# Kernel optimization log

Measured on AMD Instinct MI355X. Metric: run time of the kernel, lower is better.

Reference implementation:

```python
import jax, jax.numpy as jnp
import numpy as np

N = 100000
E = 1250000
H = 64


def setup_inputs() -> dict:
    key = jax.random.key(0)
    ks = jax.random.split(key, 20)
    x = jax.random.normal(ks[0], (N, 1), dtype=jnp.float32)
    edge_index = jax.random.randint(ks[1], (2, E), 0, N, dtype=jnp.int64)
    edge_attr = jax.random.uniform(ks[2], (E,), dtype=jnp.float32)
    def lin(k, fin, fout):
        s = 1.0 / np.sqrt(fin)
        kw, kb = jax.random.split(k)
        W = jax.random.uniform(kw, (fin, fout), minval=-s, maxval=s, dtype=jnp.float32)
        b = jax.random.uniform(kb, (fout,), minval=-s, maxval=s, dtype=jnp.float32)
        return W, b
    W1, b1 = lin(ks[3], 1, H)
    W2, b2 = lin(ks[4], H, H)
    W3, b3 = lin(ks[5], H, H)
    W4, b4 = lin(ks[6], H, H)
    W5, b5 = lin(ks[7], H, H)
    fW1, fb1 = lin(ks[8], H, H)
    fW2, fb2 = lin(ks[9], H, 1)
    return dict(x=x, edge_index=edge_index, edge_attr=edge_attr,
                W1=W1, b1=b1, W2=W2, b2=b2, W3=W3, b3=b3, W4=W4, b4=b4,
                W5=W5, b5=b5, fW1=fW1, fb1=fb1, fW2=fW2, fb2=fb2)


def _gcn_layer(x, W, b, src, dst, ew):
    # PyG GCNConv: x' = D^{-1/2}(A+I)D^{-1/2} x W + b (self-loops pre-appended)
    h = x @ W                                   # [N, H]
    deg = jax.ops.segment_sum(ew, dst, num_segments=N)
    dinv = jnp.where(deg > 0, jax.lax.rsqrt(deg), 0.0)
    norm = dinv[src] * ew * dinv[dst]           # [E+N]
    msg = h[src] * norm[:, None]                # [E+N, H]
    return jax.ops.segment_sum(msg, dst, num_segments=N) + b


def reference(x, edge_index, edge_attr, W1, b1, W2, b2, W3, b3, W4, b4, W5, b5, fW1, fb1, fW2, fb2):
    loops = jnp.arange(N, dtype=edge_index.dtype)
    src = jnp.concatenate([edge_index[0], loops])
    dst = jnp.concatenate([edge_index[1], loops])
    ew = jnp.concatenate([edge_attr, jnp.ones((N,), edge_attr.dtype)])
    h = jax.nn.relu(_gcn_layer(x, W1, b1, src, dst, ew))
    h = jax.nn.relu(_gcn_layer(h, W2, b2, src, dst, ew))
    h = jax.nn.relu(_gcn_layer(h, W3, b3, src, dst, ew))
    h = jax.nn.relu(_gcn_layer(h, W4, b4, src, dst, ew))
    h = jax.nn.relu(_gcn_layer(h, W5, b5, src, dst, ew))
    h = jax.nn.relu(h @ fW1 + fb1)
    return h @ fW2 + fb2
```

## Files before the change

kernel.cpp:

```cpp
#include <hip/hip_runtime.h>
#include <hip/hip_bf16.h>

#define NN 100000
#define EE 1250000

#define RL(x, l) __builtin_amdgcn_readlane((x), (l))
#define RLF(x, l) __int_as_float(__builtin_amdgcn_readlane(__float_as_int(x), (l)))

typedef __attribute__((ext_vector_type(8))) short v8s;
typedef __attribute__((ext_vector_type(4))) float v4f;
typedef __attribute__((ext_vector_type(4))) unsigned int v4u;

__device__ __forceinline__ unsigned short bf16rtn(float x) {
    unsigned u = __float_as_uint(x);
    unsigned r = u + 0x7fffu + ((u >> 16) & 1u);
    return (unsigned short)(r >> 16);
}
__device__ __forceinline__ unsigned bf16rtn2(float lo, float hi) {
    return (unsigned)bf16rtn(lo) | ((unsigned)bf16rtn(hi) << 16);
}
__device__ __forceinline__ float bflo(unsigned u) { return __uint_as_float(u << 16); }
__device__ __forceinline__ float bfhi(unsigned u) { return __uint_as_float(u & 0xffff0000u); }
__device__ __forceinline__ float bfs(unsigned short s) { return __uint_as_float((unsigned)s << 16); }


__global__ __launch_bounds__(256) void k_count(const int* __restrict__ ei,
                                               const float* __restrict__ ew,
                                               unsigned long long* __restrict__ cnt,
                                               int* __restrict__ slot) {
    int e = blockIdx.x * 256 + threadIdx.x;
    if (e >= EE) return;
    int d = __builtin_nontemporal_load(&ei[EE + e]);
    float w = __builtin_nontemporal_load(&ew[e]);
    unsigned fx = (unsigned)(w * 16777216.0f + 0.5f);
    unsigned long long old =
        atomicAdd(&cnt[d], (1ULL << 32) | (unsigned long long)fx);
    __builtin_nontemporal_store((int)(old >> 32), &slot[e]);
}

__global__ __launch_bounds__(256) void k_bsum(const unsigned long long* __restrict__ cnt,
                                              int* __restrict__ bsum) {
    __shared__ int ls[256];
    int b = blockIdx.x, tid = threadIdx.x;
    int base = b * 1024 + tid * 4;
    int s = 0;
    #pragma unroll
    for (int j = 0; j < 4; ++j) { int g = base + j; if (g < NN) s += (int)(cnt[g] >> 32); }
    ls[tid] = s; __syncthreads();
    for (int off = 128; off > 0; off >>= 1) {
        if (tid < off) ls[tid] += ls[tid + off];
        __syncthreads();
    }
    if (tid == 0) bsum[b] = ls[0];
}

__global__ __launch_bounds__(256) void k_scan_out(const unsigned long long* __restrict__ cnt,
                                                  const int* __restrict__ bsum,
                                                  const float* __restrict__ x,
                                                  int* __restrict__ rowptr,
                                                  float* __restrict__ dinv,
                                                  float* __restrict__ xd) {
    __shared__ int ls[256];
    __shared__ int sbase;
    int b = blockIdx.x, tid = threadIdx.x;
    if (tid < 64) {
        int w0 = (tid < b) ? bsum[tid] : 0;
        int w1 = ((64 + tid) < b) ? bsum[64 + tid] : 0;
        int s = w0 + w1;
        #pragma unroll
        for (int m = 32; m >= 1; m >>= 1) s += __shfl_xor(s, m, 64);
        if (tid == 0) sbase = s;
    }
    int base = b * 1024 + tid * 4;
    int c[4]; float sw[4]; int s = 0;
    #pragma unroll
    for (int j = 0; j < 4; ++j) {
        int g = base + j;
        unsigned long long v = (g < NN) ? cnt[g] : 0ULL;
        c[j] = (int)(v >> 32);
        sw[j] = (float)(unsigned)(v & 0xffffffffu) * (1.0f / 16777216.0f);
        s += c[j];
    }
    ls[tid] = s; __syncthreads();
    for (int off = 1; off < 256; off <<= 1) {
        int v = (tid >= off) ? ls[tid - off] : 0;
        __syncthreads();
        ls[tid] += v;
        __syncthreads();
    }
    int excl = ls[tid] - s + sbase;
    #pragma unroll
    for (int j = 0; j < 4; ++j) {
        int g = base + j;
        if (g < NN) {
            rowptr[g + 1] = excl + c[j];
            excl += c[j];
            float di = rsqrtf(sw[j] + 1.0f);
            dinv[g] = di;
            xd[g] = di * x[g];
        }
    }
    if (b == 0 && tid == 0) rowptr[0] = 0;
}

__global__ __launch_bounds__(256) void k_fill(const int* __restrict__ ei,
                                              const float* __restrict__ ew,
                                              const int* __restrict__ slot,
                                              const int* __restrict__ rowptr,
                                              int2* __restrict__ epair) {
    int e = blockIdx.x * 256 + threadIdx.x;
    if (e >= EE) return;
    int s = __builtin_nontemporal_load(&ei[e]);
    int d = __builtin_nontemporal_load(&ei[EE + e]);
    float w = __builtin_nontemporal_load(&ew[e]);
    int sl = __builtin_nontemporal_load(&slot[e]);
    int p = rowptr[d] + sl;
    epair[p] = make_int2(s, __float_as_int(w));
}

__global__ __launch_bounds__(256) void k_wpk(const float* __restrict__ Wa,
                                             const float* __restrict__ Wb,
                                             const float* __restrict__ Wc,
                                             const float* __restrict__ Wd,
                                             unsigned* __restrict__ Wf) {
    const float* W = (blockIdx.x == 0) ? Wa : (blockIdx.x == 1) ? Wb
                   : (blockIdx.x == 2) ? Wc : Wd;
    unsigned* out = Wf + blockIdx.x * 4096;
    int t = threadIdx.x;
    #pragma unroll
    for (int i = 0; i < 2; ++i) {
        int s = t * 2 + i;
        int lane = s & 63;
        int nt = (s >> 6) & 3;
        int kt = s >> 8;
        int col = nt * 16 + (lane & 15);
        int k0 = kt * 32 + (lane >> 4) * 8;
        unsigned hi[4], lo[4];
        #pragma unroll
        for (int d = 0; d < 4; ++d) {
            float w0 = W[(k0 + 2 * d) * 64 + col];
            float w1 = W[(k0 + 2 * d + 1) * 64 + col];
            unsigned short h0 = bf16rtn(w0), h1 = bf16rtn(w1);
            float r0 = w0 - bfs(h0), r1 = w1 - bfs(h1);
            hi[d] = (unsigned)h0 | ((unsigned)h1 << 16);
            lo[d] = (unsigned)bf16rtn(r0) | ((unsigned)bf16rtn(r1) << 16);
        }
        int gh = (0 * 2 + kt) * 4 + nt;
        int gl = (1 * 2 + kt) * 4 + nt;
        *(v4u*)&out[(gh * 64 + lane) * 4] = (v4u){hi[0], hi[1], hi[2], hi[3]};
        *(v4u*)&out[(gl * 64 + lane) * 4] = (v4u){lo[0], lo[1], lo[2], lo[3]};
    }
}

__device__ __forceinline__ void gatherq(
    const unsigned* __restrict__ G16, const int2* __restrict__ ep,
    int node, int beg, int end, int l16,
    float& a0, float& a1, float& a2, float& a3)
{
    uint2 su = *(const uint2*)&G16[node * 32 + l16 * 2];
    a0 = bflo(su.x); a1 = bfhi(su.x);
    a2 = bflo(su.y); a3 = bfhi(su.y);
    int j = beg;
    for (; j + 8 <= end; j += 8) {
        uint2 u[8]; float nv[8];
        #pragma unroll
        for (int t = 0; t < 8; ++t) {
            int2 p = ep[j + t];
            nv[t] = __int_as_float(p.y);
            u[t] = *(const uint2*)&G16[p.x * 32 + l16 * 2];
        }
        #pragma unroll
        for (int t = 0; t < 8; ++t) {
            a0 = fmaf(bflo(u[t].x), nv[t], a0);
            a1 = fmaf(bfhi(u[t].x), nv[t], a1);
            a2 = fmaf(bflo(u[t].y), nv[t], a2);
            a3 = fmaf(bfhi(u[t].y), nv[t], a3);
        }
    }
    if (j < end) {
        uint2 u[8]; float nv[8];
        #pragma unroll
        for (int t = 0; t < 8; ++t) {
            int idx = j + t;
            int2 p = ep[idx < end ? idx : j];
            nv[t] = (idx < end) ? __int_as_float(p.y) : 0.f;
            u[t] = *(const uint2*)&G16[p.x * 32 + l16 * 2];
        }
        #pragma unroll
        for (int t = 0; t < 8; ++t) {
            a0 = fmaf(bflo(u[t].x), nv[t], a0);
            a1 = fmaf(bfhi(u[t].x), nv[t], a1);
            a2 = fmaf(bflo(u[t].y), nv[t], a2);
            a3 = fmaf(bfhi(u[t].y), nv[t], a3);
        }
    }
}


__global__ __launch_bounds__(256) void k_l1(
    const float* __restrict__ xd, const float* __restrict__ dinv,
    const int* __restrict__ rowptr, const int2* __restrict__ ep,
    const float* __restrict__ W1, const float* __restrict__ b1,
    const float* __restrict__ W2, unsigned short* __restrict__ Gout)
{
    __shared__ float sW[4096];
    int tid = threadIdx.x;
    #pragma unroll
    for (int i = 0; i < 16; ++i) sW[tid + i * 256] = W2[tid + i * 256];
    __syncthreads();
    int lane = tid & 63, l16 = lane & 15, sub = lane >> 4;
    int g4 = blockIdx.x * 4 + (tid >> 6);
    int nodeS = g4 * 4 + sub;
    int beg = rowptr[nodeS], end = rowptr[nodeS + 1];
    float partial = 0.f;
    for (int idx = beg + l16; idx < end; idx += 16) {
        int2 p = ep[idx];
        partial = fmaf(__int_as_float(p.y), xd[p.x], partial);
    }
    #pragma unroll
    for (int m = 8; m >= 1; m >>= 1) partial += __shfl_xor(partial, m, 64);
    float z = dinv[nodeS] * (xd[nodeS] + partial);
    float z0 = RLF(z, 0), z1 = RLF(z, 16), z2 = RLF(z, 32), z3 = RLF(z, 48);
    float w1l = W1[lane], b1l = b1[lane];
    float v0 = fmaxf(fmaf(z0, w1l, b1l), 0.f);
    float v1 = fmaxf(fmaf(z1, w1l, b1l), 0.f);
    float v2 = fmaxf(fmaf(z2, w1l, b1l), 0.f);
    float v3 = fmaxf(fmaf(z3, w1l, b1l), 0.f);
    float a0 = 0.f, a1 = 0.f, a2 = 0.f, a3 = 0.f;
    #pragma unroll
    for (int k = 0; k < 64; ++k) {
        float wk = sW[k * 64 + lane];
        a0 = fmaf(RLF(v0, k), wk, a0);
        a1 = fmaf(RLF(v1, k), wk, a1);
        a2 = fmaf(RLF(v2, k), wk, a2);
        a3 = fmaf(RLF(v3, k), wk, a3);
    }
    int n0 = g4 * 4;
    Gout[(n0 + 0) * 64 + lane] = bf16rtn(dinv[n0 + 0] * a0);
    Gout[(n0 + 1) * 64 + lane] = bf16rtn(dinv[n0 + 1] * a1);
    Gout[(n0 + 2) * 64 + lane] = bf16rtn(dinv[n0 + 2] * a2);
    Gout[(n0 + 3) * 64 + lane] = bf16rtn(dinv[n0 + 3] * a3);
}

__global__ __launch_bounds__(256) void k_gmv(
    const unsigned* __restrict__ G16, const float* __restrict__ dinv,
    const int* __restrict__ rowptr, const int2* __restrict__ ep,
    const float* __restrict__ bias, const unsigned* __restrict__ Wf,
    unsigned short* __restrict__ Gout)
{
    __shared__ __align__(16) unsigned sB[4096];
    __shared__ __align__(16) unsigned sA[4][128];
    int tid = threadIdx.x;
    #pragma unroll
    for (int i = 0; i < 4; ++i)
        ((v4u*)sB)[tid + i * 256] = ((const v4u*)Wf)[tid + i * 256];
    int lane = tid & 63;
    int wid  = tid >> 6;
    int q    = lane >> 4;
    int l16  = lane & 15;
    int n0 = (blockIdx.x * 4 + wid) * 4;
    int node = n0 + q;
    int beg = rowptr[node], end = rowptr[node + 1];
    float a0, a1, a2, a3;
    gatherq(G16, ep, node, beg, end, l16, a0, a1, a2, a3);
    float din = dinv[node];
    float4 bv = *(const float4*)&bias[l16 * 4];
    float v0 = fmaxf(fmaf(din, a0, bv.x), 0.f);
    float v1 = fmaxf(fmaf(din, a1, bv.y), 0.f);
    float v2 = fmaxf(fmaf(din, a2, bv.z), 0.f);
    float v3 = fmaxf(fmaf(din, a3, bv.w), 0.f);
    *(uint2*)&sA[wid][q * 32 + l16 * 2] =
        make_uint2(bf16rtn2(v0, v1), bf16rtn2(v2, v3));
    __syncthreads();
    int rr  = lane & 3;
    int blk = lane >> 4;
    v8s fa0 = *(const v8s*)&sA[wid][rr * 32 +  0 + blk * 4];
    v8s fa1 = *(const v8s*)&sA[wid][rr * 32 + 16 + blk * 4];
    v4f acc[4];
    #pragma unroll
    for (int nt = 0; nt < 4; ++nt) {
        v8s bh0 = *(const v8s*)&sB[((0 * 4 + nt) * 64 + lane) * 4];
        v8s bh1 = *(const v8s*)&sB[((1 * 4 + nt) * 64 + lane) * 4];
        v8s bl0 = *(const v8s*)&sB[((2 * 4 + nt) * 64 + lane) * 4];
        v8s bl1 = *(const v8s*)&sB[((3 * 4 + nt) * 64 + lane) * 4];
        v4f c = {0.f, 0.f, 0.f, 0.f};
        c = __builtin_amdgcn_mfma_f32_16x16x32_bf16(fa0, bl0, c, 0, 0, 0);
        c = __builtin_amdgcn_mfma_f32_16x16x32_bf16(fa1, bl1, c, 0, 0, 0);
        c = __builtin_amdgcn_mfma_f32_16x16x32_bf16(fa0, bh0, c, 0, 0, 0);
        c = __builtin_amdgcn_mfma_f32_16x16x32_bf16(fa1, bh1, c, 0, 0, 0);
        acc[nt] = c;
    }
    if (lane < 16) {
        float4 dn = *(const float4*)&dinv[n0];
        #pragma unroll
        for (int r = 0; r < 4; ++r) {
            float d = (r == 0) ? dn.x : (r == 1) ? dn.y : (r == 2) ? dn.z : dn.w;
            #pragma unroll
            for (int nt = 0; nt < 4; ++nt)
                Gout[(n0 + r) * 64 + nt * 16 + lane] = bf16rtn(d * acc[nt][r]);
        }
    }
}

__global__ __launch_bounds__(256) void k_ghead(
    const unsigned* __restrict__ G16, const float* __restrict__ dinv,
    const int* __restrict__ rowptr, const int2* __restrict__ ep,
    const float* __restrict__ b5, const unsigned* __restrict__ Wf,
    const float* __restrict__ fb1, const float* __restrict__ fW2,
    const float* __restrict__ fb2, float* __restrict__ out)
{
    __shared__ __align__(16) unsigned sB[4096];
    __shared__ __align__(16) unsigned sA[4][128];
    int tid = threadIdx.x;
    #pragma unroll
    for (int i = 0; i < 4; ++i)
        ((v4u*)sB)[tid + i * 256] = ((const v4u*)Wf)[tid + i * 256];
    int lane = tid & 63;
    int wid  = tid >> 6;
    int q    = lane >> 4;
    int l16  = lane & 15;
    int n0 = (blockIdx.x * 4 + wid) * 4;
    int node = n0 + q;
    float fb1v[4], fw2v[4];
    #pragma unroll
    for (int nt = 0; nt < 4; ++nt) {
        fb1v[nt] = fb1[nt * 16 + l16];
        fw2v[nt] = fW2[nt * 16 + l16];
    }
    float fb2s = fb2[0];
    int beg = rowptr[node], end = rowptr[node + 1];
    float a0, a1, a2, a3;
    gatherq(G16, ep, node, beg, end, l16, a0, a1, a2, a3);
    float din = dinv[node];
    float4 bv = *(const float4*)&b5[l16 * 4];
    float v0 = fmaxf(fmaf(din, a0, bv.x), 0.f);
    float v1 = fmaxf(fmaf(din, a1, bv.y), 0.f);
    float v2 = fmaxf(fmaf(din, a2, bv.z), 0.f);
    float v3 = fmaxf(fmaf(din, a3, bv.w), 0.f);
    *(uint2*)&sA[wid][q * 32 + l16 * 2] =
        make_uint2(bf16rtn2(v0, v1), bf16rtn2(v2, v3));
    __syncthreads();
    int rr  = lane & 3;
    int blk = lane >> 4;
    v8s fa0 = *(const v8s*)&sA[wid][rr * 32 +  0 + blk * 4];
    v8s fa1 = *(const v8s*)&sA[wid][rr * 32 + 16 + blk * 4];
    v4f acc[4];
    #pragma unroll
    for (int nt = 0; nt < 4; ++nt) {
        v8s bh0 = *(const v8s*)&sB[((0 * 4 + nt) * 64 + lane) * 4];
        v8s bh1 = *(const v8s*)&sB[((1 * 4 + nt) * 64 + lane) * 4];
        v8s bl0 = *(const v8s*)&sB[((2 * 4 + nt) * 64 + lane) * 4];
        v8s bl1 = *(const v8s*)&sB[((3 * 4 + nt) * 64 + lane) * 4];
        v4f c = {0.f, 0.f, 0.f, 0.f};
        c = __builtin_amdgcn_mfma_f32_16x16x32_bf16(fa0, bl0, c, 0, 0, 0);
        c = __builtin_amdgcn_mfma_f32_16x16x32_bf16(fa1, bl1, c, 0, 0, 0);
        c = __builtin_amdgcn_mfma_f32_16x16x32_bf16(fa0, bh0, c, 0, 0, 0);
        c = __builtin_amdgcn_mfma_f32_16x16x32_bf16(fa1, bh1, c, 0, 0, 0);
        acc[nt] = c;
    }
    float tr[4];
    #pragma unroll
    for (int r = 0; r < 4; ++r) {
        float t = 0.f;
        #pragma unroll
        for (int nt = 0; nt < 4; ++nt)
            t += fmaxf(acc[nt][r] + fb1v[nt], 0.f) * fw2v[nt];
        #pragma unroll
        for (int m = 8; m >= 1; m >>= 1) t += __shfl_xor(t, m, 64);
        tr[r] = t;
    }
    if (lane == 0) {
        float4 o = {tr[0] + fb2s, tr[1] + fb2s, tr[2] + fb2s, tr[3] + fb2s};
        *(float4*)&out[n0] = o;
    }
}


extern "C" void kernel_launch(void* const* d_in, const int* in_sizes, int n_in,
                              void* d_out, int out_size, void* d_ws, size_t ws_size,
                              hipStream_t stream) {
    const float* x   = (const float*)d_in[0];
    const int*   ei  = (const int*)d_in[1];
    const float* ew  = (const float*)d_in[2];
    const float* W1  = (const float*)d_in[3];
    const float* b1  = (const float*)d_in[4];
    const float* W2  = (const float*)d_in[5];
    const float* b2  = (const float*)d_in[6];
    const float* W3  = (const float*)d_in[7];
    const float* b3  = (const float*)d_in[8];
    const float* W4  = (const float*)d_in[9];
    const float* b4  = (const float*)d_in[10];
    const float* W5  = (const float*)d_in[11];
    const float* b5  = (const float*)d_in[12];
    const float* fW1 = (const float*)d_in[13];
    const float* fb1 = (const float*)d_in[14];
    const float* fW2 = (const float*)d_in[15];
    const float* fb2 = (const float*)d_in[16];
    float* out = (float*)d_out;

    char* ws = (char*)d_ws;
    size_t o = 0;
    auto alloc = [&](size_t elems) -> void* {
        void* p = (void*)(ws + o);
        o += ((elems * 4 + 255) / 256) * 256;
        return p;
    };
    float* dinv   = (float*)alloc(NN);
    float* xd     = (float*)alloc(NN);
    int*   rowptr = (int*)alloc(NN + 1);
    unsigned long long* cnt64 = (unsigned long long*)alloc(2 * (size_t)NN);
    int*   bsum   = (int*)alloc(128);
    int2*  epair  = (int2*)alloc(2 * (size_t)EE);
    unsigned* Ga16 = (unsigned*)alloc((size_t)NN * 32);
    unsigned* Gb16 = (unsigned*)alloc((size_t)NN * 32);
    int*   slot   = (int*)alloc(EE);
    unsigned* Wf  = (unsigned*)alloc(4 * 4096);

    int gE  = (EE + 255) / 256;
    int nb  = (NN + 1023) / 1024;
    int gW4 = NN / 16;

    k_wpk<<<4, 256, 0, stream>>>(W3, W4, W5, fW1, Wf);
    hipMemsetAsync(cnt64, 0, NN * sizeof(unsigned long long), stream);
    k_count<<<gE, 256, 0, stream>>>(ei, ew, cnt64, slot);
    k_bsum<<<nb, 256, 0, stream>>>(cnt64, bsum);
    k_scan_out<<<nb, 256, 0, stream>>>(cnt64, bsum, x, rowptr, dinv, xd);
    k_fill<<<gE, 256, 0, stream>>>(ei, ew, slot, rowptr, epair);

    k_l1<<<gW4, 256, 0, stream>>>(xd, dinv, rowptr, epair, W1, b1, W2,
                                  (unsigned short*)Ga16);
    k_gmv<<<gW4, 256, 0, stream>>>(Ga16, dinv, rowptr, epair, b2, Wf + 0,
                                   (unsigned short*)Gb16);
    k_gmv<<<gW4, 256, 0, stream>>>(Gb16, dinv, rowptr, epair, b3, Wf + 4096,
                                   (unsigned short*)Ga16);
    k_gmv<<<gW4, 256, 0, stream>>>(Ga16, dinv, rowptr, epair, b4, Wf + 8192,
                                   (unsigned short*)Gb16);
    k_ghead<<<gW4, 256, 0, stream>>>(Gb16, dinv, rowptr, epair, b5, Wf + 12288,
                                     fb1, fW2, fb2, out);
}
```

Measured before the change: 399.7 us.

## Gather 8 nodes per wavefront with 16-byte row loads in GCN layers

```diff
diff --git a/kernel.cpp b/kernel.cpp
--- a/kernel.cpp
+++ b/kernel.cpp
@@ -152,46 +152,55 @@
     }
 }
 
-__device__ __forceinline__ void gatherq(
+__device__ __forceinline__ void gatherq8(
     const unsigned* __restrict__ G16, const int2* __restrict__ ep,
-    int node, int beg, int end, int l16,
-    float& a0, float& a1, float& a2, float& a3)
+    int node, int beg, int end, int l8, float a[8])
 {
-    uint2 su = *(const uint2*)&G16[node * 32 + l16 * 2];
-    a0 = bflo(su.x); a1 = bfhi(su.x);
-    a2 = bflo(su.y); a3 = bfhi(su.y);
+    uint4 su = *(const uint4*)&G16[node * 32 + l8 * 4];
+    a[0] = bflo(su.x); a[1] = bfhi(su.x);
+    a[2] = bflo(su.y); a[3] = bfhi(su.y);
+    a[4] = bflo(su.z); a[5] = bfhi(su.z);
+    a[6] = bflo(su.w); a[7] = bfhi(su.w);
     int j = beg;
     for (; j + 8 <= end; j += 8) {
-        uint2 u[8]; float nv[8];
+        uint4 u[8]; float nv[8];
         #pragma unroll
         for (int t = 0; t < 8; ++t) {
             int2 p = ep[j + t];
             nv[t] = __int_as_float(p.y);
-            u[t] = *(const uint2*)&G16[p.x * 32 + l16 * 2];
+            u[t] = *(const uint4*)&G16[p.x * 32 + l8 * 4];
         }
         #pragma unroll
         for (int t = 0; t < 8; ++t) {
-            a0 = fmaf(bflo(u[t].x), nv[t], a0);
-            a1 = fmaf(bfhi(u[t].x), nv[t], a1);
-            a2 = fmaf(bflo(u[t].y), nv[t], a2);
-            a3 = fmaf(bfhi(u[t].y), nv[t], a3);
+            a[0] = fmaf(bflo(u[t].x), nv[t], a[0]);
+            a[1] = fmaf(bfhi(u[t].x), nv[t], a[1]);
+            a[2] = fmaf(bflo(u[t].y), nv[t], a[2]);
+            a[3] = fmaf(bfhi(u[t].y), nv[t], a[3]);
+            a[4] = fmaf(bflo(u[t].z), nv[t], a[4]);
+            a[5] = fmaf(bfhi(u[t].z), nv[t], a[5]);
+            a[6] = fmaf(bflo(u[t].w), nv[t], a[6]);
+            a[7] = fmaf(bfhi(u[t].w), nv[t], a[7]);
         }
     }
     if (j < end) {
-        uint2 u[8]; float nv[8];
+        uint4 u[8]; float nv[8];
         #pragma unroll
         for (int t = 0; t < 8; ++t) {
             int idx = j + t;
             int2 p = ep[idx < end ? idx : j];
             nv[t] = (idx < end) ? __int_as_float(p.y) : 0.f;
-            u[t] = *(const uint2*)&G16[p.x * 32 + l16 * 2];
+            u[t] = *(const uint4*)&G16[p.x * 32 + l8 * 4];
         }
         #pragma unroll
         for (int t = 0; t < 8; ++t) {
-            a0 = fmaf(bflo(u[t].x), nv[t], a0);
-            a1 = fmaf(bfhi(u[t].x), nv[t], a1);
-            a2 = fmaf(bflo(u[t].y), nv[t], a2);
-            a3 = fmaf(bfhi(u[t].y), nv[t], a3);
+            a[0] = fmaf(bflo(u[t].x), nv[t], a[0]);
+            a[1] = fmaf(bfhi(u[t].x), nv[t], a[1]);
+            a[2] = fmaf(bflo(u[t].y), nv[t], a[2]);
+            a[3] = fmaf(bfhi(u[t].y), nv[t], a[3]);
+            a[4] = fmaf(bflo(u[t].z), nv[t], a[4]);
+            a[5] = fmaf(bfhi(u[t].z), nv[t], a[5]);
+            a[6] = fmaf(bflo(u[t].w), nv[t], a[6]);
+            a[7] = fmaf(bfhi(u[t].w), nv[t], a[7]);
         }
     }
 }
@@ -249,30 +258,36 @@
     unsigned short* __restrict__ Gout)
 {
     __shared__ __align__(16) unsigned sB[4096];
-    __shared__ __align__(16) unsigned sA[4][128];
+    __shared__ __align__(16) unsigned sA[4][256];
     int tid = threadIdx.x;
     #pragma unroll
     for (int i = 0; i < 4; ++i)
         ((v4u*)sB)[tid + i * 256] = ((const v4u*)Wf)[tid + i * 256];
     int lane = tid & 63;
     int wid  = tid >> 6;
-    int q    = lane >> 4;
-    int l16  = lane & 15;
-    int n0 = (blockIdx.x * 4 + wid) * 4;
+    int q    = lane >> 3;
+    int l8   = lane & 7;
+    int n0 = (blockIdx.x * 4 + wid) * 8;
     int node = n0 + q;
     int beg = rowptr[node], end = rowptr[node + 1];
-    float a0, a1, a2, a3;
-    gatherq(G16, ep, node, beg, end, l16, a0, a1, a2, a3);
+    float a[8];
+    gatherq8(G16, ep, node, beg, end, l8, a);
     float din = dinv[node];
-    float4 bv = *(const float4*)&bias[l16 * 4];
-    float v0 = fmaxf(fmaf(din, a0, bv.x), 0.f);
-    float v1 = fmaxf(fmaf(din, a1, bv.y), 0.f);
-    float v2 = fmaxf(fmaf(din, a2, bv.z), 0.f);
-    float v3 = fmaxf(fmaf(din, a3, bv.w), 0.f);
-    *(uint2*)&sA[wid][q * 32 + l16 * 2] =
-        make_uint2(bf16rtn2(v0, v1), bf16rtn2(v2, v3));
+    float4 bv0 = ((const float4*)bias)[l8 * 2];
+    float4 bv1 = ((const float4*)bias)[l8 * 2 + 1];
+    float v0 = fmaxf(fmaf(din, a[0], bv0.x), 0.f);
+    float v1 = fmaxf(fmaf(din, a[1], bv0.y), 0.f);
+    float v2 = fmaxf(fmaf(din, a[2], bv0.z), 0.f);
+    float v3 = fmaxf(fmaf(din, a[3], bv0.w), 0.f);
+    float v4 = fmaxf(fmaf(din, a[4], bv1.x), 0.f);
+    float v5 = fmaxf(fmaf(din, a[5], bv1.y), 0.f);
+    float v6 = fmaxf(fmaf(din, a[6], bv1.z), 0.f);
+    float v7 = fmaxf(fmaf(din, a[7], bv1.w), 0.f);
+    *(uint4*)&sA[wid][q * 32 + l8 * 4] = make_uint4(
+        bf16rtn2(v0, v1), bf16rtn2(v2, v3),
+        bf16rtn2(v4, v5), bf16rtn2(v6, v7));
     __syncthreads();
-    int rr  = lane & 3;
+    int rr  = lane & 7;
     int blk = lane >> 4;
     v8s fa0 = *(const v8s*)&sA[wid][rr * 32 +  0 + blk * 4];
     v8s fa1 = *(const v8s*)&sA[wid][rr * 32 + 16 + blk * 4];
@@ -290,14 +305,17 @@
         c = __builtin_amdgcn_mfma_f32_16x16x32_bf16(fa1, bh1, c, 0, 0, 0);
         acc[nt] = c;
     }
-    if (lane < 16) {
-        float4 dn = *(const float4*)&dinv[n0];
+    int grp = lane >> 4;
+    int l16 = lane & 15;
+    if (grp < 2) {
+        int rb = grp * 4;
+        float4 dn = *(const float4*)&dinv[n0 + rb];
         #pragma unroll
         for (int r = 0; r < 4; ++r) {
             float d = (r == 0) ? dn.x : (r == 1) ? dn.y : (r == 2) ? dn.z : dn.w;
             #pragma unroll
             for (int nt = 0; nt < 4; ++nt)
-                Gout[(n0 + r) * 64 + nt * 16 + lane] = bf16rtn(d * acc[nt][r]);
+                Gout[(n0 + rb + r) * 64 + nt * 16 + l16] = bf16rtn(d * acc[nt][r]);
         }
     }
 }
@@ -310,16 +328,17 @@
     const float* __restrict__ fb2, float* __restrict__ out)
 {
     __shared__ __align__(16) unsigned sB[4096];
-    __shared__ __align__(16) unsigned sA[4][128];
+    __shared__ __align__(16) unsigned sA[4][256];
     int tid = threadIdx.x;
     #pragma unroll
     for (int i = 0; i < 4; ++i)
         ((v4u*)sB)[tid + i * 256] = ((const v4u*)Wf)[tid + i * 256];
     int lane = tid & 63;
     int wid  = tid >> 6;
-    int q    = lane >> 4;
+    int q    = lane >> 3;
+    int l8   = lane & 7;
     int l16  = lane & 15;
-    int n0 = (blockIdx.x * 4 + wid) * 4;
+    int n0 = (blockIdx.x * 4 + wid) * 8;
     int node = n0 + q;
     float fb1v[4], fw2v[4];
     #pragma unroll
@@ -329,18 +348,24 @@
     }
     float fb2s = fb2[0];
     int beg = rowptr[node], end = rowptr[node + 1];
-    float a0, a1, a2, a3;
-    gatherq(G16, ep, node, beg, end, l16, a0, a1, a2, a3);
+    float a[8];
+    gatherq8(G16, ep, node, beg, end, l8, a);
     float din = dinv[node];
-    float4 bv = *(const float4*)&b5[l16 * 4];
-    float v0 = fmaxf(fmaf(din, a0, bv.x), 0.f);
-    float v1 = fmaxf(fmaf(din, a1, bv.y), 0.f);
-    float v2 = fmaxf(fmaf(din, a2, bv.z), 0.f);
-    float v3 = fmaxf(fmaf(din, a3, bv.w), 0.f);
-    *(uint2*)&sA[wid][q * 32 + l16 * 2] =
-        make_uint2(bf16rtn2(v0, v1), bf16rtn2(v2, v3));
+    float4 bv0 = ((const float4*)b5)[l8 * 2];
+    float4 bv1 = ((const float4*)b5)[l8 * 2 + 1];
+    float v0 = fmaxf(fmaf(din, a[0], bv0.x), 0.f);
+    float v1 = fmaxf(fmaf(din, a[1], bv0.y), 0.f);
+    float v2 = fmaxf(fmaf(din, a[2], bv0.z), 0.f);
+    float v3 = fmaxf(fmaf(din, a[3], bv0.w), 0.f);
+    float v4 = fmaxf(fmaf(din, a[4], bv1.x), 0.f);
+    float v5 = fmaxf(fmaf(din, a[5], bv1.y), 0.f);
+    float v6 = fmaxf(fmaf(din, a[6], bv1.z), 0.f);
+    float v7 = fmaxf(fmaf(din, a[7], bv1.w), 0.f);
+    *(uint4*)&sA[wid][q * 32 + l8 * 4] = make_uint4(
+        bf16rtn2(v0, v1), bf16rtn2(v2, v3),
+        bf16rtn2(v4, v5), bf16rtn2(v6, v7));
     __syncthreads();
-    int rr  = lane & 3;
+    int rr  = lane & 7;
     int blk = lane >> 4;
     v8s fa0 = *(const v8s*)&sA[wid][rr * 32 +  0 + blk * 4];
     v8s fa1 = *(const v8s*)&sA[wid][rr * 32 + 16 + blk * 4];
@@ -372,6 +397,9 @@
     if (lane == 0) {
         float4 o = {tr[0] + fb2s, tr[1] + fb2s, tr[2] + fb2s, tr[3] + fb2s};
         *(float4*)&out[n0] = o;
+    } else if (lane == 16) {
+        float4 o = {tr[0] + fb2s, tr[1] + fb2s, tr[2] + fb2s, tr[3] + fb2s};
+        *(float4*)&out[n0 + 4] = o;
     }
 }
 
@@ -419,6 +447,7 @@
     int gE  = (EE + 255) / 256;
     int nb  = (NN + 1023) / 1024;
     int gW4 = NN / 16;
+    int gW8 = NN / 32;
 
     k_wpk<<<4, 256, 0, stream>>>(W3, W4, W5, fW1, Wf);
     hipMemsetAsync(cnt64, 0, NN * sizeof(unsigned long long), stream);
@@ -429,12 +458,12 @@
 
     k_l1<<<gW4, 256, 0, stream>>>(xd, dinv, rowptr, epair, W1, b1, W2,
                                   (unsigned short*)Ga16);
-    k_gmv<<<gW4, 256, 0, stream>>>(Ga16, dinv, rowptr, epair, b2, Wf + 0,
+    k_gmv<<<gW8, 256, 0, stream>>>(Ga16, dinv, rowptr, epair, b2, Wf + 0,
                                    (unsigned short*)Gb16);
-    k_gmv<<<gW4, 256, 0, stream>>>(Gb16, dinv, rowptr, epair, b3, Wf + 4096,
+    k_gmv<<<gW8, 256, 0, stream>>>(Gb16, dinv, rowptr, epair, b3, Wf + 4096,
                                    (unsigned short*)Ga16);
-    k_gmv<<<gW4, 256, 0, stream>>>(Ga16, dinv, rowptr, epair, b4, Wf + 8192,
+    k_gmv<<<gW8, 256, 0, stream>>>(Ga16, dinv, rowptr, epair, b4, Wf + 8192,
                                    (unsigned short*)Gb16);
-    k_ghead<<<gW4, 256, 0, stream>>>(Gb16, dinv, rowptr, epair, b5, Wf + 12288,
+    k_ghead<<<gW8, 256, 0, stream>>>(Gb16, dinv, rowptr, epair, b5, Wf + 12288,
                                      fb1, fW2, fb2, out);
 }
```

Result: faster. 367.0 us (-8.2%).
